# Kernel optimization log

Hardware: AMD Instinct MI355X
Metric: run time of the kernel (lower is better)

## Reference

```python
import jax, jax.numpy as jnp
import numpy as np

DIM = 1024
NUM_HEADS = 16
HEAD_DIM = DIM // NUM_HEADS
SCALE = HEAD_DIM ** (-0.5)


def setup_inputs() -> dict:
    key = jax.random.key(0)
    ks = jax.random.split(key, 5)
    B, L, D = 2, 2048, DIM
    x = jax.random.normal(ks[0], (B, L, D), dtype=jnp.float32)
    # torch nn.Linear init scale ~ U(-1/sqrt(fan_in), 1/sqrt(fan_in)); use small normals
    s = 1.0 / np.sqrt(D)
    qkv_w = jax.random.uniform(ks[1], (3 * D, D), minval=-s, maxval=s, dtype=jnp.float32)
    qkv_b = jax.random.uniform(ks[2], (3 * D,), minval=-s, maxval=s, dtype=jnp.float32)
    proj_w = jax.random.uniform(ks[3], (D, D), minval=-s, maxval=s, dtype=jnp.float32)
    proj_b = jax.random.uniform(ks[4], (D,), minval=-s, maxval=s, dtype=jnp.float32)
    return {"x": x, "qkv_w": qkv_w, "qkv_b": qkv_b, "proj_w": proj_w, "proj_b": proj_b}


def reference(x, qkv_w, qkv_b, proj_w, proj_b):
    B, L, D = x.shape
    H, Hd = NUM_HEADS, HEAD_DIM
    # QKV projection: [B,L,3D] -> [3,B,H,L,Hd]
    qkv = x @ qkv_w.T + qkv_b
    qkv = qkv.reshape(B, L, 3, H, Hd).transpose(2, 0, 3, 1, 4)
    q, k, v = qkv[0], qkv[1], qkv[2]
    scores = jnp.einsum('bhqd,bhkd->bhqk', q, k) * SCALE  # [B,H,L,L]
    attn = jax.nn.softmax(scores, axis=-1)
    out = jnp.einsum('bhqk,bhkd->bhqd', attn, v)  # [B,H,L,Hd]
    out = out.transpose(0, 2, 1, 3).reshape(B, L, D)
    out = out @ proj_w.T + proj_b
    return out
```

## Files before the change

### kernel.cpp

```cpp
#include <hip/hip_runtime.h>
#include <hip/hip_bf16.h>
#include <cstdint>
#include <cstddef>

#define D_MODEL 1024
#define NHEADS 16
#define HD 64
#define NB 2
#define SL 2048
#define SEQ (NB*SL)
#define NQKV (3*D_MODEL)

typedef __attribute__((ext_vector_type(8))) short short8;
typedef __attribute__((ext_vector_type(4))) float floatx4;
typedef __attribute__((ext_vector_type(16))) float f32x16;
typedef unsigned short u16;

__device__ __forceinline__ u16 f2bf(float f) {
    union { float f; uint32_t u; } v; v.f = f;
    return (u16)((v.u + 0x7fffu + ((v.u >> 16) & 1u)) >> 16);
}

__device__ __forceinline__ uint32_t cvt_pk_bf16(float lo, float hi) {
    uint32_t r;
    asm("v_cvt_pk_bf16_f32 %0, %1, %2" : "=v"(r) : "v"(lo), "v"(hi));
    return r;
}

__device__ __forceinline__ void pl32swap(uint32_t &a, uint32_t &b) {
    asm("v_permlane32_swap_b32 %0, %1" : "+v"(a), "+v"(b));
}

__device__ __forceinline__ float exp2f_fast(float x) {
    float r; asm("v_exp_f32 %0, %1" : "=v"(r) : "v"(x)); return r;
}

__device__ __forceinline__ float m3f(float a, float b, float c) {
    return fmaxf(fmaxf(a, b), c);
}

__device__ __forceinline__ float vmax16(const f32x16& v) {
    float a0 = m3f(v[0], v[1], v[2]);
    float a1 = m3f(v[3], v[4], v[5]);
    float a2 = m3f(v[6], v[7], v[8]);
    float a3 = m3f(v[9], v[10], v[11]);
    float a4 = m3f(v[12], v[13], v[14]);
    return fmaxf(m3f(a0, a1, v[15]), m3f(a2, a3, a4));
}

__device__ __forceinline__ f32x16 zero16() {
    f32x16 z;
    #pragma unroll
    for (int i = 0; i < 16; i++) z[i] = 0.f;
    return z;
}

#define GLDS(gsrc, ldst) __builtin_amdgcn_global_load_lds( \
    (const __attribute__((address_space(1))) void*)(gsrc), \
    (__attribute__((address_space(3))) void*)(ldst), 16, 0, 0)

__global__ __launch_bounds__(256) void cvt_all(const float* __restrict__ x,
                                               const float* __restrict__ w1,
                                               const float* __restrict__ w2,
                                               u16* __restrict__ xb,
                                               u16* __restrict__ w1b,
                                               u16* __restrict__ w2b) {
    int i = blockIdx.x * 256 + threadIdx.x;
    const float4* src; ushort4* dst; int j;
    if (i < 1048576)      { src = (const float4*)x;  dst = (ushort4*)xb;  j = i; }
    else if (i < 1835008) { src = (const float4*)w1; dst = (ushort4*)w1b; j = i - 1048576; }
    else                  { src = (const float4*)w2; dst = (ushort4*)w2b; j = i - 1835008; }
    float4 f = src[j];
    ushort4 o;
    o.x = f2bf(f.x); o.y = f2bf(f.y); o.z = f2bf(f.z); o.w = f2bf(f.w);
    dst[j] = o;
}

__device__ __forceinline__ void gemm128_dbuf(const u16* __restrict__ A,
                                             const u16* __restrict__ B,
                                             int mbase, int nbase, int K,
                                             u16* Alds, u16* Blds,
                                             floatx4 acc[4][4]) {
    const int tid = threadIdx.x;
    const int lane = tid & 63;
    const int l15 = lane & 15, quad = lane >> 4;
    const int wave = tid >> 6;
    const int wr = wave >> 1, wc = wave & 1;
    #pragma unroll
    for (int i = 0; i < 4; i++)
        #pragma unroll
        for (int j = 0; j < 4; j++)
            acc[i][j] = (floatx4){0.f, 0.f, 0.f, 0.f};

    const int r0 = tid >> 2, kg0 = (tid & 3) * 8;
    const u16* Arow0 = A + (size_t)(mbase + r0) * K + kg0;
    const u16* Arow1 = A + (size_t)(mbase + r0 + 64) * K + kg0;
    const u16* Brow0 = B + (size_t)(nbase + r0) * K + kg0;
    const u16* Brow1 = B + (size_t)(nbase + r0 + 64) * K + kg0;

    GLDS(Arow0, Alds + tid * 8);
    GLDS(Arow1, Alds + (256 + tid) * 8);
    GLDS(Brow0, Blds + tid * 8);
    GLDS(Brow1, Blds + (256 + tid) * 8);
    __syncthreads();

    const int NT = K >> 5;
    for (int t = 0; t < NT; t++) {
        const int cur = t & 1;
        if (t + 1 < NT) {
            const int k0 = (t + 1) << 5;
            u16* Ad = Alds + (cur ^ 1) * 4096;
            u16* Bd = Blds + (cur ^ 1) * 4096;
            GLDS(Arow0 + k0, Ad + tid * 8);
            GLDS(Arow1 + k0, Ad + (256 + tid) * 8);
            GLDS(Brow0 + k0, Bd + tid * 8);
            GLDS(Brow1 + k0, Bd + (256 + tid) * 8);
        }
        const u16* Ac = Alds + cur * 4096;
        const u16* Bc = Blds + cur * 4096;
        short8 af[4], bf[4];
        #pragma unroll
        for (int i = 0; i < 4; i++)
            af[i] = *(const short8*)(Ac + (wr * 64 + i * 16 + l15) * 32 + quad * 8);
        #pragma unroll
        for (int j = 0; j < 4; j++)
            bf[j] = *(const short8*)(Bc + (wc * 64 + j * 16 + l15) * 32 + quad * 8);
        #pragma unroll
        for (int i = 0; i < 4; i++)
            #pragma unroll
            for (int j = 0; j < 4; j++)
                acc[i][j] = __builtin_amdgcn_mfma_f32_16x16x32_bf16(af[i], bf[j], acc[i][j], 0, 0, 0);
        __syncthreads();
    }
}

__global__ __launch_bounds__(256) void qkv_gemm(const u16* __restrict__ xb,
                                                const u16* __restrict__ wb,
                                                const float* __restrict__ bias,
                                                u16* __restrict__ Qo, u16* __restrict__ Ko,
                                                u16* __restrict__ Vt) {
    __shared__ __align__(16) u16 Alds[2 * 128 * 32];
    __shared__ __align__(16) u16 Blds[2 * 128 * 32];
    const int mbase = blockIdx.y * 128;
    const int nbase = blockIdx.x * 128;
    floatx4 acc[4][4];
    gemm128_dbuf(xb, wb, mbase, nbase, 1024, Alds, Blds, acc);
    const int lane = threadIdx.x & 63;
    const int wave = threadIdx.x >> 6;
    const int wr = wave >> 1, wc = wave & 1;
    const int l15 = lane & 15, quad = lane >> 4;
    const int which = nbase >> 10;
    #pragma unroll
    for (int j = 0; j < 4; j++) {
        int n = nbase + wc * 64 + j * 16 + l15;
        float bv = bias[n];
        int within = n & 1023;
        int h = within >> 6, d = within & 63;
        #pragma unroll
        for (int i = 0; i < 4; i++) {
            int m0 = mbase + wr * 64 + i * 16 + quad * 4;
            int b = m0 >> 11;
            int bh = b * NHEADS + h;
            if (which == 2) {
                int l0 = m0 & 2047;
                int slot = ((l0 >> 5) & 1) * 256 + ((l0 >> 4) & 1) * 128 + (d >> 5) * 64 + ((l0 >> 3) & 1) * 32 + (d & 31);
                ushort4 pk;
                pk.x = f2bf(acc[i][j][0] + bv); pk.y = f2bf(acc[i][j][1] + bv);
                pk.z = f2bf(acc[i][j][2] + bv); pk.w = f2bf(acc[i][j][3] + bv);
                *(ushort4*)(Vt + (size_t)bh * (SL * HD) + (size_t)(l0 >> 6) * 4096 + slot * 8 + (l0 & 7)) = pk;
            } else {
                #pragma unroll
                for (int r = 0; r < 4; r++) {
                    int m = m0 + r;
                    int l = m & 2047;
                    float v = acc[i][j][r] + bv;
                    if (which == 0) {
                        Qo[((size_t)bh * SL + l) * HD + d] = f2bf(v * 0.18033688f);
                    } else {
                        int slot = ((l >> 5) & 1) * 256 + (d >> 4) * 64 + ((d >> 3) & 1) * 32 + (l & 31);
                        Ko[(size_t)bh * (SL * HD) + (size_t)(l >> 6) * 4096 + slot * 8 + (d & 7)] = f2bf(v);
                    }
                }
            }
        }
    }
}

__global__ __launch_bounds__(256, 2) void flash_kernel(const u16* __restrict__ Q,
                                                       const u16* __restrict__ K,
                                                       const u16* __restrict__ V,
                                                       u16* __restrict__ AO) {
    __shared__ __align__(16) u16 Klds[2 * 4096];
    __shared__ __align__(16) u16 Vlds[2 * 4096];
    const int tid = threadIdx.x;
    const int lane = tid & 63;
    const int wave = tid >> 6;
    const int hi = lane >> 5;
    const int l31 = lane & 31;
    const int lane8 = lane * 8;

    const int bid = (int)blockIdx.x;
    const int swz = (bid & 7) * 64 + (bid >> 3);
    const int bh = swz >> 4;
    const int qb = swz & 15;
    const int b = bh >> 4, h = bh & 15;
    const int qbase = qb * 128 + wave * 32;

    const u16* Qp = Q + (size_t)bh * SL * HD;
    const u16* Kg = K + (size_t)bh * (SL * HD);
    const u16* Vg = V + (size_t)bh * (SL * HD);

    short8 qf[4];
    #pragma unroll
    for (int c = 0; c < 4; c++)
        qf[c] = *(const short8*)(Qp + (size_t)(qbase + l31) * HD + c * 16 + hi * 8);

    f32x16 accO0 = zero16(), accO1 = zero16();
    float m_i = -__builtin_inff();
    float l_i = 0.f;

    GLDS(Kg + tid * 8,         Klds + tid * 8);
    GLDS(Kg + (256 + tid) * 8, Klds + (256 + tid) * 8);
    GLDS(Vg + tid * 8,         Vlds + tid * 8);
    GLDS(Vg + (256 + tid) * 8, Vlds + (256 + tid) * 8);
    __syncthreads();

    union PW { uint32_t w[4]; short8 s8; };

    for (int t = 0; t < SL / 64; t++) {
        const int cur = t & 1;
        if (t + 1 < SL / 64) {
            const u16* ks = Kg + (size_t)(t + 1) * 4096;
            const u16* vs = Vg + (size_t)(t + 1) * 4096;
            u16* kd = Klds + (cur ^ 1) * 4096;
            u16* vd = Vlds + (cur ^ 1) * 4096;
            GLDS(ks + tid * 8,         kd + tid * 8);
            GLDS(ks + (256 + tid) * 8, kd + (256 + tid) * 8);
            GLDS(vs + tid * 8,         vd + tid * 8);
            GLDS(vs + (256 + tid) * 8, vd + (256 + tid) * 8);
        }
        const u16* Kt  = Klds + cur * 4096;
        const u16* Vt_ = Vlds + cur * 4096;

        f32x16 sA = zero16(), sB = zero16();
        __builtin_amdgcn_s_setprio(1);
        #pragma unroll
        for (int c = 0; c < 4; c++) {
            short8 kf = *(const short8*)(Kt + c * 512 + lane8);
            sA = __builtin_amdgcn_mfma_f32_32x32x16_bf16(kf, qf[c], sA, 0, 0, 0);
        }
        #pragma unroll
        for (int c = 0; c < 4; c++) {
            short8 kf = *(const short8*)(Kt + 2048 + c * 512 + lane8);
            sB = __builtin_amdgcn_mfma_f32_32x32x16_bf16(kf, qf[c], sB, 0, 0, 0);
        }
        __builtin_amdgcn_s_setprio(0);

        float pmax = fmaxf(vmax16(sA), vmax16(sB));
        if (!__all(pmax - m_i <= 24.0f)) {
            float mo = m_i;
            float mn = fmaxf(mo, fmaxf(pmax, __shfl_xor(pmax, 32, 64)));
            m_i = mn;
            float alpha = exp2f_fast(mo - mn);
            l_i *= alpha;
            #pragma unroll
            for (int e = 0; e < 16; e++) { accO0[e] *= alpha; accO1[e] *= alpha; }
        }
        #pragma unroll
        for (int e = 0; e < 16; e++) sA[e] = exp2f_fast(sA[e] - m_i);
        #pragma unroll
        for (int e = 0; e < 16; e++) sB[e] = exp2f_fast(sB[e] - m_i);
        float r0 = 0.f, r1 = 0.f, r2 = 0.f, r3 = 0.f;
        #pragma unroll
        for (int e = 0; e < 16; e += 4) {
            r0 += sA[e]; r1 += sA[e + 1]; r2 += sA[e + 2]; r3 += sA[e + 3];
        }
        #pragma unroll
        for (int e = 0; e < 16; e += 4) {
            r0 += sB[e]; r1 += sB[e + 1]; r2 += sB[e + 2]; r3 += sB[e + 3];
        }
        float rs = (r0 + r1) + (r2 + r3);
        rs += __shfl_xor(rs, 32, 64);
        l_i += rs;

#define PV_SUB(SV, OFF) { \
        uint32_t a0 = cvt_pk_bf16(SV[0], SV[1]);  uint32_t b0 = cvt_pk_bf16(SV[4], SV[5]);  pl32swap(a0, b0); \
        uint32_t a1 = cvt_pk_bf16(SV[2], SV[3]);  uint32_t b1 = cvt_pk_bf16(SV[6], SV[7]);  pl32swap(a1, b1); \
        PW f0; f0.w[0] = a0; f0.w[1] = a1; f0.w[2] = b0; f0.w[3] = b1; \
        accO0 = __builtin_amdgcn_mfma_f32_32x32x16_bf16(*(const short8*)(Vt_ + (OFF) + lane8),        f0.s8, accO0, 0, 0, 0); \
        accO1 = __builtin_amdgcn_mfma_f32_32x32x16_bf16(*(const short8*)(Vt_ + (OFF) + 512 + lane8),  f0.s8, accO1, 0, 0, 0); \
        uint32_t c0 = cvt_pk_bf16(SV[8], SV[9]);  uint32_t d0 = cvt_pk_bf16(SV[12], SV[13]); pl32swap(c0, d0); \
        uint32_t c1 = cvt_pk_bf16(SV[10], SV[11]); uint32_t d1 = cvt_pk_bf16(SV[14], SV[15]); pl32swap(c1, d1); \
        PW f1; f1.w[0] = c0; f1.w[1] = c1; f1.w[2] = d0; f1.w[3] = d1; \
        accO0 = __builtin_amdgcn_mfma_f32_32x32x16_bf16(*(const short8*)(Vt_ + (OFF) + 1024 + lane8),       f1.s8, accO0, 0, 0, 0); \
        accO1 = __builtin_amdgcn_mfma_f32_32x32x16_bf16(*(const short8*)(Vt_ + (OFF) + 1024 + 512 + lane8), f1.s8, accO1, 0, 0, 0); }

        __builtin_amdgcn_s_setprio(1);
        PV_SUB(sA, 0);
        PV_SUB(sB, 2048);
        __builtin_amdgcn_s_setprio(0);
#undef PV_SUB

        __syncthreads();
    }

    const float invl = 1.f / l_i;
    const int qrow = qbase + l31;
    const size_t rowbase = ((size_t)(b * SL + qrow)) * D_MODEL + h * HD;
    #pragma unroll
    for (int rg = 0; rg < 4; rg++) {
        ushort4 o0, o1;
        o0.x = f2bf(accO0[rg * 4 + 0] * invl); o0.y = f2bf(accO0[rg * 4 + 1] * invl);
        o0.z = f2bf(accO0[rg * 4 + 2] * invl); o0.w = f2bf(accO0[rg * 4 + 3] * invl);
        *(ushort4*)(AO + rowbase + rg * 8 + 4 * hi) = o0;
        o1.x = f2bf(accO1[rg * 4 + 0] * invl); o1.y = f2bf(accO1[rg * 4 + 1] * invl);
        o1.z = f2bf(accO1[rg * 4 + 2] * invl); o1.w = f2bf(accO1[rg * 4 + 3] * invl);
        *(ushort4*)(AO + rowbase + 32 + rg * 8 + 4 * hi) = o1;
    }
}

__global__ __launch_bounds__(256) void proj_gemm(const u16* __restrict__ ab,
                                                 const u16* __restrict__ wb,
                                                 const float* __restrict__ bias,
                                                 float* __restrict__ out) {
    __shared__ __align__(16) u16 Alds[2 * 128 * 32];
    __shared__ __align__(16) u16 Blds[2 * 128 * 32];
    const int mbase = blockIdx.y * 128;
    const int nbase = blockIdx.x * 128;
    floatx4 acc[4][4];
    gemm128_dbuf(ab, wb, mbase, nbase, 1024, Alds, Blds, acc);
    const int lane = threadIdx.x & 63;
    const int wave = threadIdx.x >> 6;
    const int wr = wave >> 1, wc = wave & 1;
    const int l15 = lane & 15, quad = lane >> 4;
    #pragma unroll
    for (int j = 0; j < 4; j++) {
        int n = nbase + wc * 64 + j * 16 + l15;
        float bv = bias[n];
        #pragma unroll
        for (int i = 0; i < 4; i++) {
            #pragma unroll
            for (int r = 0; r < 4; r++) {
                int m = mbase + wr * 64 + i * 16 + quad * 4 + r;
                out[(size_t)m * D_MODEL + n] = acc[i][j][r] + bv;
            }
        }
    }
}

extern "C" void kernel_launch(void* const* d_in, const int* in_sizes, int n_in,
                              void* d_out, int out_size, void* d_ws, size_t ws_size,
                              hipStream_t stream) {
    const float* x      = (const float*)d_in[0];
    const float* qkv_w  = (const float*)d_in[1];
    const float* qkv_b  = (const float*)d_in[2];
    const float* proj_w = (const float*)d_in[3];
    const float* proj_b = (const float*)d_in[4];
    float* out = (float*)d_out;
    char* ws = (char*)d_ws;

    u16* xb    = (u16*)(ws);
    u16* wqkv  = (u16*)(ws + 8388608);
    u16* wproj = (u16*)(ws + 14680064);
    u16* Qb    = (u16*)(ws + 16777216);
    u16* Kb    = (u16*)(ws + 25165824);
    u16* Vt    = (u16*)(ws + 33554432);
    u16* AO    = (u16*)(ws + 41943040);

    cvt_all<<<8192, 256, 0, stream>>>(x, qkv_w, proj_w, xb, wqkv, wproj);
    qkv_gemm<<<dim3(NQKV / 128, SEQ / 128), 256, 0, stream>>>(xb, wqkv, qkv_b, Qb, Kb, Vt);
    flash_kernel<<<dim3(512), 256, 0, stream>>>(Qb, Kb, Vt, AO);
    proj_gemm<<<dim3(D_MODEL / 128, SEQ / 128), 256, 0, stream>>>(AO, wproj, proj_b, out);
}
```

Before: 198.6 us.

## Split KV sequence across two wave groups in flash kernel and merge partials

The flash attention block grows from 256 to 512 threads. Two groups of four waves each process half of the KV sequence for the same 128 query rows, using separate double-buffered LDS regions. At the end, the second group writes its partial accumulators and softmax stats to LDS, and the first group merges them with log-sum-exp rescaling before writing output. This doubles the waves per block to hide latency, at the cost of more LDS per block, an extra reduction step, and possibly lower occupancy in blocks per CU.

```diff
diff --git a/kernel.cpp b/kernel.cpp
--- a/kernel.cpp
+++ b/kernel.cpp
@@ -186,15 +186,17 @@
     }
 }
 
-__global__ __launch_bounds__(256, 2) void flash_kernel(const u16* __restrict__ Q,
+__global__ __launch_bounds__(512, 4) void flash_kernel(const u16* __restrict__ Q,
                                                        const u16* __restrict__ K,
                                                        const u16* __restrict__ V,
                                                        u16* __restrict__ AO) {
-    __shared__ __align__(16) u16 Klds[2 * 4096];
-    __shared__ __align__(16) u16 Vlds[2 * 4096];
+    __shared__ __align__(16) u16 smem[32768];
     const int tid = threadIdx.x;
     const int lane = tid & 63;
     const int wave = tid >> 6;
+    const int qc = wave & 3;
+    const int kvh = wave >> 2;
+    const int tl = tid & 255;
     const int hi = lane >> 5;
     const int l31 = lane & 31;
     const int lane8 = lane * 8;
@@ -203,12 +205,15 @@
     const int swz = (bid & 7) * 64 + (bid >> 3);
     const int bh = swz >> 4;
     const int qb = swz & 15;
-    const int b = bh >> 4, h = bh & 15;
-    const int qbase = qb * 128 + wave * 32;
+    const int b = bh >> 4, hd = bh & 15;
+    const int qbase = qb * 128 + qc * 32;
 
     const u16* Qp = Q + (size_t)bh * SL * HD;
-    const u16* Kg = K + (size_t)bh * (SL * HD);
-    const u16* Vg = V + (size_t)bh * (SL * HD);
+    const u16* Kg = K + (size_t)bh * (SL * HD) + (size_t)kvh * 16 * 4096;
+    const u16* Vg = V + (size_t)bh * (SL * HD) + (size_t)kvh * 16 * 4096;
+
+    u16* Kb_ = smem + kvh * 16384;
+    u16* Vb_ = smem + kvh * 16384 + 8192;
 
     short8 qf[4];
     #pragma unroll
@@ -219,28 +224,29 @@
     float m_i = -__builtin_inff();
     float l_i = 0.f;
 
-    GLDS(Kg + tid * 8,         Klds + tid * 8);
-    GLDS(Kg + (256 + tid) * 8, Klds + (256 + tid) * 8);
-    GLDS(Vg + tid * 8,         Vlds + tid * 8);
-    GLDS(Vg + (256 + tid) * 8, Vlds + (256 + tid) * 8);
+    GLDS(Kg + tl * 8,         Kb_ + tl * 8);
+    GLDS(Kg + (256 + tl) * 8, Kb_ + (256 + tl) * 8);
+    GLDS(Vg + tl * 8,         Vb_ + tl * 8);
+    GLDS(Vg + (256 + tl) * 8, Vb_ + (256 + tl) * 8);
     __syncthreads();
 
     union PW { uint32_t w[4]; short8 s8; };
 
-    for (int t = 0; t < SL / 64; t++) {
+    #pragma unroll 1
+    for (int t = 0; t < 16; t++) {
         const int cur = t & 1;
-        if (t + 1 < SL / 64) {
+        if (t + 1 < 16) {
             const u16* ks = Kg + (size_t)(t + 1) * 4096;
             const u16* vs = Vg + (size_t)(t + 1) * 4096;
-            u16* kd = Klds + (cur ^ 1) * 4096;
-            u16* vd = Vlds + (cur ^ 1) * 4096;
-            GLDS(ks + tid * 8,         kd + tid * 8);
-            GLDS(ks + (256 + tid) * 8, kd + (256 + tid) * 8);
-            GLDS(vs + tid * 8,         vd + tid * 8);
-            GLDS(vs + (256 + tid) * 8, vd + (256 + tid) * 8);
-        }
-        const u16* Kt  = Klds + cur * 4096;
-        const u16* Vt_ = Vlds + cur * 4096;
+            u16* kd = Kb_ + (cur ^ 1) * 4096;
+            u16* vd = Vb_ + (cur ^ 1) * 4096;
+            GLDS(ks + tl * 8,         kd + tl * 8);
+            GLDS(ks + (256 + tl) * 8, kd + (256 + tl) * 8);
+            GLDS(vs + tl * 8,         vd + tl * 8);
+            GLDS(vs + (256 + tl) * 8, vd + (256 + tl) * 8);
+        }
+        const u16* Kt  = Kb_ + cur * 4096;
+        const u16* Vt_ = Vb_ + cur * 4096;
 
         f32x16 sA = zero16(), sB = zero16();
         __builtin_amdgcn_s_setprio(1);
@@ -304,18 +310,36 @@
         __syncthreads();
     }
 
-    const float invl = 1.f / l_i;
-    const int qrow = qbase + l31;
-    const size_t rowbase = ((size_t)(b * SL + qrow)) * D_MODEL + h * HD;
-    #pragma unroll
-    for (int rg = 0; rg < 4; rg++) {
-        ushort4 o0, o1;
-        o0.x = f2bf(accO0[rg * 4 + 0] * invl); o0.y = f2bf(accO0[rg * 4 + 1] * invl);
-        o0.z = f2bf(accO0[rg * 4 + 2] * invl); o0.w = f2bf(accO0[rg * 4 + 3] * invl);
-        *(ushort4*)(AO + rowbase + rg * 8 + 4 * hi) = o0;
-        o1.x = f2bf(accO1[rg * 4 + 0] * invl); o1.y = f2bf(accO1[rg * 4 + 1] * invl);
-        o1.z = f2bf(accO1[rg * 4 + 2] * invl); o1.w = f2bf(accO1[rg * 4 + 3] * invl);
-        *(ushort4*)(AO + rowbase + 32 + rg * 8 + 4 * hi) = o1;
+    float* xch = (float*)smem;
+    if (kvh) {
+        float* p = xch + (qc * 64 + lane) * 35;
+        #pragma unroll
+        for (int e = 0; e < 16; e++) { p[e] = accO0[e]; p[16 + e] = accO1[e]; }
+        p[32] = m_i; p[33] = l_i;
+    }
+    __syncthreads();
+    if (!kvh) {
+        const float* p = xch + (qc * 64 + lane) * 35;
+        float mB = p[32], lB = p[33];
+        float m = fmaxf(m_i, mB);
+        float s0 = exp2f_fast(m_i - m);
+        float s1 = exp2f_fast(mB - m);
+        float inv = 1.f / (s0 * l_i + s1 * lB);
+        const size_t rowbase = ((size_t)(b * SL + qbase + l31)) * D_MODEL + hd * HD;
+        #pragma unroll
+        for (int rg = 0; rg < 4; rg++) {
+            ushort4 o0, o1;
+            o0.x = f2bf((s0 * accO0[rg * 4 + 0] + s1 * p[rg * 4 + 0]) * inv);
+            o0.y = f2bf((s0 * accO0[rg * 4 + 1] + s1 * p[rg * 4 + 1]) * inv);
+            o0.z = f2bf((s0 * accO0[rg * 4 + 2] + s1 * p[rg * 4 + 2]) * inv);
+            o0.w = f2bf((s0 * accO0[rg * 4 + 3] + s1 * p[rg * 4 + 3]) * inv);
+            *(ushort4*)(AO + rowbase + rg * 8 + 4 * hi) = o0;
+            o1.x = f2bf((s0 * accO1[rg * 4 + 0] + s1 * p[16 + rg * 4 + 0]) * inv);
+            o1.y = f2bf((s0 * accO1[rg * 4 + 1] + s1 * p[16 + rg * 4 + 1]) * inv);
+            o1.z = f2bf((s0 * accO1[rg * 4 + 2] + s1 * p[16 + rg * 4 + 2]) * inv);
+            o1.w = f2bf((s0 * accO1[rg * 4 + 3] + s1 * p[16 + rg * 4 + 3]) * inv);
+            *(ushort4*)(AO + rowbase + 32 + rg * 8 + 4 * hi) = o1;
+        }
     }
 }
 
@@ -369,6 +393,6 @@
 
     cvt_all<<<8192, 256, 0, stream>>>(x, qkv_w, proj_w, xb, wqkv, wproj);
     qkv_gemm<<<dim3(NQKV / 128, SEQ / 128), 256, 0, stream>>>(xb, wqkv, qkv_b, Qb, Kb, Vt);
-    flash_kernel<<<dim3(512), 256, 0, stream>>>(Qb, Kb, Vt, AO);
+    flash_kernel<<<dim3(512), 512, 0, stream>>>(Qb, Kb, Vt, AO);
     proj_gemm<<<dim3(D_MODEL / 128, SEQ / 128), 256, 0, stream>>>(AO, wproj, proj_b, out);
 }
```

Measured after the change: 196.8 us. About the same (-0.9%).
